# Kernel tuning notes

Measured on AMD Instinct MI355X. Metric: run time of the kernel, lower is better.

The kernel has to match this reference:

```python
import jax, jax.numpy as jnp
import numpy as np

NUM_HEADS = 8

def setup_inputs() -> dict:
    key = jax.random.key(0)
    kq, kk, kv = jax.random.split(key, 3)
    shape = (8, 12, 512, 256)  # (batch, in_steps, num_nodes, model_dim)
    return {
        "query": jax.random.normal(kq, shape, dtype=jnp.float32),
        "key": jax.random.normal(kk, shape, dtype=jnp.float32),
        "value": jax.random.normal(kv, shape, dtype=jnp.float32),
    }

def reference(query, key, value):
    # torch split(dim=-1)/cat(dim=0) == reshape feature dim into (H, head_dim)
    # contiguous chunks; heads stay independent so math matches standard MHA.
    B, T, Nq, D = query.shape
    Nk = key.shape[-2]
    H = NUM_HEADS
    d = D // H
    q = query.reshape(B, T, Nq, H, d)
    k = key.reshape(B, T, Nk, H, d)
    v = value.reshape(B, T, Nk, H, d)
    # scores: (B, T, H, Nq, Nk)
    scores = jnp.einsum("btqhd,btkhd->bthqk", q, k) / jnp.sqrt(jnp.asarray(d, q.dtype))
    attn = jax.nn.softmax(scores, axis=-1)
    out = jnp.einsum("bthqk,btkhd->btqhd", attn, v)
    return out.reshape(B, T, Nq, D)
```

## Files before the change

kernel.cpp:

```cpp
#include <hip/hip_runtime.h>
#include <hip/hip_bf16.h>


#define N_    512
#define DM    256
#define DH    32
#define CHUNK 512

typedef __attribute__((ext_vector_type(8))) short bf16x8;
typedef __attribute__((ext_vector_type(4))) float f32x4;

__device__ __forceinline__ unsigned short f2bf(float f) {
    unsigned int u = __builtin_bit_cast(unsigned int, f);
    return (unsigned short)((u + 0x8000u) >> 16);
}

__device__ __forceinline__ unsigned int pack_hi16(float a, float b) {
    return __builtin_amdgcn_perm(__builtin_bit_cast(unsigned int, b),
                                 __builtin_bit_cast(unsigned int, a),
                                 0x07060302u);
}

__device__ __forceinline__ unsigned int pack_lo16(unsigned int lo, unsigned int hi) {
    return __builtin_amdgcn_perm(hi, lo, 0x05040100u);
}

__device__ __forceinline__ int fxor(int d) {
    return ((d >> 2) ^ ((d & 3) << 1)) & 7;
}

__global__ __launch_bounds__(1024, 4) void attn_mha_kernel(
    const float* __restrict__ Q, const float* __restrict__ K,
    const float* __restrict__ V, float* __restrict__ O)
{
    __shared__ unsigned short kls[CHUNK * DH];
    __shared__ unsigned short vtls[DH * CHUNK];

    const int tid = threadIdx.x;
    const int wave = tid >> 6;
    const int lane = tid & 63;
    const int lr = lane & 15;
    const int lh = lane >> 4;

    const float QSC = 32.64105756f;
    const int kslot = (lh ^ ((lr >> 1) & 3)) * 8;

    bf16x8 ones;
    #pragma unroll
    for (int i = 0; i < 8; ++i) ones[i] = (short)0x3F80;

    const f32x4 minit = {14714.92f, 14714.92f, 14714.92f, 14714.92f};

    #pragma unroll 1
    for (int hh = 0; hh < 3; ++hh) {
        const int f  = blockIdx.x * 3 + hh;
        const int bt = f >> 3;
        const int h  = f & 7;
        const size_t base = (size_t)bt * (N_ * DM) + (size_t)h * DH;
        const float* Qg = Q + base;
        const float* Kg = K + base;
        const float* Vg = V + base;
        float*       Og = O + base;

        bf16x8 qf[2];
        #pragma unroll
        for (int t = 0; t < 2; ++t) {
            const int q0 = wave * 32 + t * 16;
            const float* qp = Qg + (size_t)(q0 + lr) * DM + lh * 8;
            const float4 qa = *(const float4*)qp;
            const float4 qb = *(const float4*)(qp + 4);
            bf16x8 q;
            q[0] = (short)f2bf(qa.x * QSC); q[1] = (short)f2bf(qa.y * QSC);
            q[2] = (short)f2bf(qa.z * QSC); q[3] = (short)f2bf(qa.w * QSC);
            q[4] = (short)f2bf(qb.x * QSC); q[5] = (short)f2bf(qb.y * QSC);
            q[6] = (short)f2bf(qb.z * QSC); q[7] = (short)f2bf(qb.w * QSC);
            qf[t] = q;
        }

        if (hh) __syncthreads();

        {
            const int d4 = tid & 7;
            const int r0 = tid >> 3;
            #pragma unroll 2
            for (int p = 0; p < 4; ++p) {
                const int kvl = p * 128 + r0;
                const float4 kf = *(const float4*)(Kg + (size_t)kvl * DM + d4 * 4);
                const int slot = (d4 >> 1) ^ ((kvl >> 1) & 3);
                ushort4 w;
                w.x = f2bf(kf.x); w.y = f2bf(kf.y); w.z = f2bf(kf.z); w.w = f2bf(kf.w);
                *(ushort4*)(&kls[kvl * 32 + slot * 8 + (d4 & 1) * 4]) = w;
            }
            #pragma unroll 2
            for (int p = 0; p < 2; ++p) {
                const int m = p * 128 + r0;
                const int grp = m >> 4;
                const int w   = m & 15;
                const int kvl = grp * 32 + ((w & 1) << 4) + ((w >> 1) << 1);
                const float* vp = Vg + (size_t)kvl * DM + d4 * 4;
                const float4 a = *(const float4*)vp;
                const float4 b = *(const float4*)(vp + DM);
                const float av[4] = {a.x, a.y, a.z, a.w};
                const float bv[4] = {b.x, b.y, b.z, b.w};
                const int pp  = ((kvl >> 2) & 3) * 8 + ((kvl >> 4) & 1) * 4 + (kvl & 3);
                const int idx = (kvl & ~31) + pp;
                const int g  = idx >> 3;
                const int go = idx & 7;
                #pragma unroll
                for (int i = 0; i < 4; ++i) {
                    const int d = d4 * 4 + i;
                    const unsigned int pk = pack_hi16(av[i], bv[i]);
                    *(unsigned int*)(&vtls[d * CHUNK + (g ^ fxor(d)) * 8 + go]) = pk;
                }
            }
        }
        __syncthreads();

        f32x4 o0[2], o1[2], lsa[2];
        #pragma unroll
        for (int t = 0; t < 2; ++t) {
            o0[t]  = (f32x4){0.f, 0.f, 0.f, 0.f};
            o1[t]  = (f32x4){0.f, 0.f, 0.f, 0.f};
            lsa[t] = (f32x4){0.f, 0.f, 0.f, 0.f};
        }

        #pragma unroll 1
        for (int it = 0; it < 16; ++it) {
            const int c0 = it * 32;

            const bf16x8 kb0 = *(const bf16x8*)(&kls[(c0 + lr) * 32 + kslot]);
            const bf16x8 kb1 = *(const bf16x8*)(&kls[(c0 + 16 + lr) * 32 + kslot]);
            const int G = it * 4 + lh;
            const bf16x8 vb0 = *(const bf16x8*)(&vtls[lr * CHUNK + (G ^ fxor(lr)) * 8]);
            const bf16x8 vb1 = *(const bf16x8*)(&vtls[(16 + lr) * CHUNK + (G ^ fxor(16 + lr)) * 8]);

            #pragma unroll
            for (int t = 0; t < 2; ++t) {
                f32x4 s0 = __builtin_amdgcn_mfma_f32_16x16x32_bf16(kb0, qf[t], minit, 0, 0, 0);
                f32x4 s1 = __builtin_amdgcn_mfma_f32_16x16x32_bf16(kb1, qf[t], minit, 0, 0, 0);

                unsigned int e00 = (unsigned int)(int)s0[0];
                unsigned int e01 = (unsigned int)(int)s0[1];
                unsigned int e02 = (unsigned int)(int)s0[2];
                unsigned int e03 = (unsigned int)(int)s0[3];
                unsigned int e10 = (unsigned int)(int)s1[0];
                unsigned int e11 = (unsigned int)(int)s1[1];
                unsigned int e12 = (unsigned int)(int)s1[2];
                unsigned int e13 = (unsigned int)(int)s1[3];

                union { unsigned int w[4]; bf16x8 v; } pa;
                pa.w[0] = pack_lo16(e00, e01);
                pa.w[1] = pack_lo16(e02, e03);
                pa.w[2] = pack_lo16(e10, e11);
                pa.w[3] = pack_lo16(e12, e13);

                lsa[t] = __builtin_amdgcn_mfma_f32_16x16x32_bf16(pa.v, ones, lsa[t], 0, 0, 0);
                o0[t]  = __builtin_amdgcn_mfma_f32_16x16x32_bf16(pa.v, vb0, o0[t], 0, 0, 0);
                o1[t]  = __builtin_amdgcn_mfma_f32_16x16x32_bf16(pa.v, vb1, o1[t], 0, 0, 0);
            }
        }

        #pragma unroll
        for (int t = 0; t < 2; ++t) {
            #pragma unroll
            for (int r = 0; r < 4; ++r) {
                const float inv = 1.0f / lsa[t][r];
                float* orow = Og + (size_t)(wave * 32 + t * 16 + lh * 4 + r) * DM;
                orow[lr]      = o0[t][r] * inv;
                orow[16 + lr] = o1[t][r] * inv;
            }
        }
    }
}

extern "C" void kernel_launch(void* const* d_in, const int* in_sizes, int n_in,
                              void* d_out, int out_size, void* d_ws, size_t ws_size,
                              hipStream_t stream) {
    const float* Q = (const float*)d_in[0];
    const float* K = (const float*)d_in[1];
    const float* V = (const float*)d_in[2];
    float* O = (float*)d_out;
    attn_mha_kernel<<<dim3(256), dim3(1024), 0, stream>>>(Q, K, V, O);
}
```

Before: 52.54 us.

## Split query rows across blocks of 512 threads and reuse staged K/V

Each block now has 512 threads and handles half the query rows of a head per unit of work. The grid doubles to 512 blocks, and each block processes 3 half-heads. K/V staging into LDS is skipped when consecutive units share the same head, so the stage is reused. The score MFMAs for both query tiles are also issued before the exp/pack step, giving more independent MFMA work to overlap. Each block now stages K/V with half the threads. Because the units per block are odd, one head's K/V is staged twice, once by each of two adjacent blocks.

```diff
diff --git a/kernel.cpp b/kernel.cpp
--- a/kernel.cpp
+++ b/kernel.cpp
@@ -29,7 +29,7 @@
     return ((d >> 2) ^ ((d & 3) << 1)) & 7;
 }
 
-__global__ __launch_bounds__(1024, 4) void attn_mha_kernel(
+__global__ __launch_bounds__(512, 4) void attn_mha_kernel(
     const float* __restrict__ Q, const float* __restrict__ K,
     const float* __restrict__ V, float* __restrict__ O)
 {
@@ -51,11 +51,15 @@
 
     const f32x4 minit = {14714.92f, 14714.92f, 14714.92f, 14714.92f};
 
+    int staged = -1;
+
     #pragma unroll 1
-    for (int hh = 0; hh < 3; ++hh) {
-        const int f  = blockIdx.x * 3 + hh;
-        const int bt = f >> 3;
-        const int h  = f & 7;
+    for (int u = 0; u < 3; ++u) {
+        const int hidx = blockIdx.x * 3 + u;
+        const int f    = hidx >> 1;
+        const int qh   = hidx & 1;
+        const int bt   = f >> 3;
+        const int h    = f & 7;
         const size_t base = (size_t)bt * (N_ * DM) + (size_t)h * DH;
         const float* Qg = Q + base;
         const float* Kg = K + base;
@@ -65,7 +69,7 @@
         bf16x8 qf[2];
         #pragma unroll
         for (int t = 0; t < 2; ++t) {
-            const int q0 = wave * 32 + t * 16;
+            const int q0 = qh * 256 + wave * 32 + t * 16;
             const float* qp = Qg + (size_t)(q0 + lr) * DM + lh * 8;
             const float4 qa = *(const float4*)qp;
             const float4 qb = *(const float4*)(qp + 4);
@@ -77,14 +81,13 @@
             qf[t] = q;
         }
 
-        if (hh) __syncthreads();
-
-        {
+        if (f != staged) {
+            if (staged >= 0) __syncthreads();
             const int d4 = tid & 7;
             const int r0 = tid >> 3;
             #pragma unroll 2
-            for (int p = 0; p < 4; ++p) {
-                const int kvl = p * 128 + r0;
+            for (int p = 0; p < 8; ++p) {
+                const int kvl = p * 64 + r0;
                 const float4 kf = *(const float4*)(Kg + (size_t)kvl * DM + d4 * 4);
                 const int slot = (d4 >> 1) ^ ((kvl >> 1) & 3);
                 ushort4 w;
@@ -92,8 +95,8 @@
                 *(ushort4*)(&kls[kvl * 32 + slot * 8 + (d4 & 1) * 4]) = w;
             }
             #pragma unroll 2
-            for (int p = 0; p < 2; ++p) {
-                const int m = p * 128 + r0;
+            for (int p = 0; p < 4; ++p) {
+                const int m = p * 64 + r0;
                 const int grp = m >> 4;
                 const int w   = m & 15;
                 const int kvl = grp * 32 + ((w & 1) << 4) + ((w >> 1) << 1);
@@ -113,8 +116,9 @@
                     *(unsigned int*)(&vtls[d * CHUNK + (g ^ fxor(d)) * 8 + go]) = pk;
                 }
             }
+            staged = f;
+            __syncthreads();
         }
-        __syncthreads();
 
         f32x4 o0[2], o1[2], lsa[2];
         #pragma unroll
@@ -134,19 +138,22 @@
             const bf16x8 vb0 = *(const bf16x8*)(&vtls[lr * CHUNK + (G ^ fxor(lr)) * 8]);
             const bf16x8 vb1 = *(const bf16x8*)(&vtls[(16 + lr) * CHUNK + (G ^ fxor(16 + lr)) * 8]);
 
+            f32x4 s0[2], s1[2];
             #pragma unroll
             for (int t = 0; t < 2; ++t) {
-                f32x4 s0 = __builtin_amdgcn_mfma_f32_16x16x32_bf16(kb0, qf[t], minit, 0, 0, 0);
-                f32x4 s1 = __builtin_amdgcn_mfma_f32_16x16x32_bf16(kb1, qf[t], minit, 0, 0, 0);
-
-                unsigned int e00 = (unsigned int)(int)s0[0];
-                unsigned int e01 = (unsigned int)(int)s0[1];
-                unsigned int e02 = (unsigned int)(int)s0[2];
-                unsigned int e03 = (unsigned int)(int)s0[3];
-                unsigned int e10 = (unsigned int)(int)s1[0];
-                unsigned int e11 = (unsigned int)(int)s1[1];
-                unsigned int e12 = (unsigned int)(int)s1[2];
-                unsigned int e13 = (unsigned int)(int)s1[3];
+                s0[t] = __builtin_amdgcn_mfma_f32_16x16x32_bf16(kb0, qf[t], minit, 0, 0, 0);
+                s1[t] = __builtin_amdgcn_mfma_f32_16x16x32_bf16(kb1, qf[t], minit, 0, 0, 0);
+            }
+            #pragma unroll
+            for (int t = 0; t < 2; ++t) {
+                unsigned int e00 = (unsigned int)(int)s0[t][0];
+                unsigned int e01 = (unsigned int)(int)s0[t][1];
+                unsigned int e02 = (unsigned int)(int)s0[t][2];
+                unsigned int e03 = (unsigned int)(int)s0[t][3];
+                unsigned int e10 = (unsigned int)(int)s1[t][0];
+                unsigned int e11 = (unsigned int)(int)s1[t][1];
+                unsigned int e12 = (unsigned int)(int)s1[t][2];
+                unsigned int e13 = (unsigned int)(int)s1[t][3];
 
                 union { unsigned int w[4]; bf16x8 v; } pa;
                 pa.w[0] = pack_lo16(e00, e01);
@@ -165,7 +172,7 @@
             #pragma unroll
             for (int r = 0; r < 4; ++r) {
                 const float inv = 1.0f / lsa[t][r];
-                float* orow = Og + (size_t)(wave * 32 + t * 16 + lh * 4 + r) * DM;
+                float* orow = Og + (size_t)(qh * 256 + wave * 32 + t * 16 + lh * 4 + r) * DM;
                 orow[lr]      = o0[t][r] * inv;
                 orow[16 + lr] = o1[t][r] * inv;
             }
@@ -180,5 +187,5 @@
     const float* K = (const float*)d_in[1];
     const float* V = (const float*)d_in[2];
     float* O = (float*)d_out;
-    attn_mha_kernel<<<dim3(256), dim3(1024), 0, stream>>>(Q, K, V, O);
+    attn_mha_kernel<<<dim3(512), dim3(512), 0, stream>>>(Q, K, V, O);
 }
```

New measurement: 51.30 us. 1.02x faster.
